# Performance work log

Hardware: AMD Instinct MI355X
Metric: run time of the kernel (lower is better)

The kernel has to match this reference:

```python
import jax, jax.numpy as jnp
import numpy as np

N_NODES = 50000
N_EDGES = 800000
IN_DIM = 128
OUT_DIM = 256


def setup_inputs() -> dict:
    key = jax.random.key(0)
    k1, k2, k3, k4 = jax.random.split(key, 4)
    feat = jax.random.normal(k1, (N_NODES, IN_DIM), dtype=jnp.float32)
    # xavier_uniform with relu gain, shape [in_dim, out_dim] (applied as h @ W)
    gain = np.sqrt(2.0)
    bound = gain * np.sqrt(6.0 / (IN_DIM + OUT_DIM))
    W = jax.random.uniform(k2, (IN_DIM, OUT_DIM), dtype=jnp.float32,
                           minval=-bound, maxval=bound)
    src = jax.random.randint(k3, (N_EDGES,), 0, N_NODES, dtype=jnp.int64)
    dst = jax.random.randint(k4, (N_EDGES,), 0, N_NODES, dtype=jnp.int64)
    return {"feat": feat, "W": W, "src": src, "dst": dst}


def reference(feat, W, src, dst):
    n = feat.shape[0]
    # mean aggregation over incoming neighbors (copy_src + mean on dst)
    msg_sum = jax.ops.segment_sum(feat[src], dst, num_segments=n)  # [N, in_dim]
    deg = jax.ops.segment_sum(jnp.ones_like(dst, dtype=feat.dtype), dst,
                              num_segments=n)  # [N]
    h_neigh = msg_sum / jnp.maximum(deg, 1.0)[:, None]  # zero-degree -> 0
    # self_loop=False path: fc((feat + h_neigh) / 2), then relu
    h = ((feat + h_neigh) * 0.5) @ W  # [N, out_dim]
    return jax.nn.relu(h)
```

## Files before the change

### kernel.cpp

```cpp
#include <hip/hip_runtime.h>
#include <hip/hip_fp16.h>

#define N_NODES 50000
#define N_EDGES 800000
#define IN_DIM  128
#define OUT_DIM 256
#define SCAN_BLOCKS ((N_NODES + 255) / 256)
#define WT_STRIDE 136

typedef _Float16 f16x8 __attribute__((ext_vector_type(8)));
typedef _Float16 f16x4 __attribute__((ext_vector_type(4)));
typedef float f32x4 __attribute__((ext_vector_type(4)));

__global__ void probe_idx_dtype(const int* __restrict__ words,
                                int* __restrict__ flag) {
  __shared__ int cnt;
  if (threadIdx.x == 0) cnt = 0;
  __syncthreads();
  int j = 2 * (int)threadIdx.x + 1;
  if (words[j] != 0) atomicAdd(&cnt, 1);
  __syncthreads();
  if (threadIdx.x == 0) *flag = (cnt == 0) ? 1 : 0;
}

__device__ __forceinline__ long idx_off(long e, int flag) {
  return flag ? (e << 1) : e;
}

__global__ __launch_bounds__(256) void hist_kernel(
    const int* __restrict__ dst, const int* __restrict__ flag,
    int* __restrict__ hist) {
  int e = blockIdx.x * 256 + threadIdx.x;
  if (e >= N_EDGES) return;
  int d = dst[idx_off(e, *flag)];
  atomicAdd(&hist[d], 1);
}

__global__ __launch_bounds__(256) void scan_block(
    const int* __restrict__ hist, int* __restrict__ pre,
    int* __restrict__ bsum) {
  __shared__ int s[256];
  int tid = threadIdx.x;
  int i = blockIdx.x * 256 + tid;
  int v = (i < N_NODES) ? hist[i] : 0;
  s[tid] = v;
  __syncthreads();
  for (int off = 1; off < 256; off <<= 1) {
    int t = (tid >= off) ? s[tid - off] : 0;
    __syncthreads();
    s[tid] += t;
    __syncthreads();
  }
  if (i < N_NODES) pre[i] = s[tid] - v;
  if (tid == 255) bsum[blockIdx.x] = s[255];
}

__global__ __launch_bounds__(256) void scan_tops(int* __restrict__ bsum) {
  __shared__ int s[256];
  int tid = threadIdx.x;
  int v = (tid < SCAN_BLOCKS) ? bsum[tid] : 0;
  s[tid] = v;
  __syncthreads();
  for (int off = 1; off < 256; off <<= 1) {
    int t = (tid >= off) ? s[tid - off] : 0;
    __syncthreads();
    s[tid] += t;
    __syncthreads();
  }
  if (tid < SCAN_BLOCKS) bsum[tid] = s[tid] - v;
}

__global__ __launch_bounds__(256) void scan_add(
    const int* __restrict__ pre, const int* __restrict__ bsum,
    int* __restrict__ row_start) {
  int i = blockIdx.x * 256 + threadIdx.x;
  if (i < N_NODES) row_start[i] = pre[i] + bsum[blockIdx.x];
  if (i == 0) row_start[N_NODES] = N_EDGES;
}

__global__ __launch_bounds__(256) void scatter_kernel(
    const int* __restrict__ src, const int* __restrict__ dst,
    const int* __restrict__ flag, const int* __restrict__ row_start,
    int* __restrict__ cursor, int* __restrict__ esrc) {
  int e = blockIdx.x * 256 + threadIdx.x;
  if (e >= N_EDGES) return;
  int f = *flag;
  int d = dst[idx_off(e, f)];
  int s = src[idx_off(e, f)];
  int pos = row_start[d] + atomicAdd(&cursor[d], 1);
  esrc[pos] = s;
}

__global__ __launch_bounds__(256) void cast_feat(
    const float* __restrict__ feat, __half* __restrict__ feat16) {
  size_t i = ((size_t)blockIdx.x * 256 + threadIdx.x) * 8;
  float4 v0 = *reinterpret_cast<const float4*>(feat + i);
  float4 v1 = *reinterpret_cast<const float4*>(feat + i + 4);
  __half2 h[4];
  h[0] = __floats2half2_rn(v0.x, v0.y);
  h[1] = __floats2half2_rn(v0.z, v0.w);
  h[2] = __floats2half2_rn(v1.x, v1.y);
  h[3] = __floats2half2_rn(v1.z, v1.w);
  *reinterpret_cast<float4*>(feat16 + i) = *reinterpret_cast<float4*>(h);
}

__global__ __launch_bounds__(256) void aggregate_f32(
    const float* __restrict__ feat, const int* __restrict__ esrc,
    const int* __restrict__ row_start, __half2* __restrict__ x) {
  int node = blockIdx.x * 4 + ((int)threadIdx.x >> 6);
  int lane = (int)threadIdx.x & 63;
  if (node >= N_NODES) return;
  int rs = row_start[node];
  int re = row_start[node + 1];
  float2 a0 = {0.f, 0.f}, a1 = {0.f, 0.f};
  int e = rs;
  for (; e + 1 < re; e += 2) {
    int s0 = esrc[e];
    int s1 = esrc[e + 1];
    float2 v0 = *reinterpret_cast<const float2*>(feat + (size_t)s0 * IN_DIM + lane * 2);
    float2 v1 = *reinterpret_cast<const float2*>(feat + (size_t)s1 * IN_DIM + lane * 2);
    a0.x += v0.x; a0.y += v0.y;
    a1.x += v1.x; a1.y += v1.y;
  }
  if (e < re) {
    int s0 = esrc[e];
    float2 v0 = *reinterpret_cast<const float2*>(feat + (size_t)s0 * IN_DIM + lane * 2);
    a0.x += v0.x; a0.y += v0.y;
  }
  float deg = (float)(re - rs);
  float rdeg = (deg > 0.f) ? 1.0f / deg : 0.0f;
  float2 f = *reinterpret_cast<const float2*>(feat + (size_t)node * IN_DIM + lane * 2);
  float x0 = (f.x + (a0.x + a1.x) * rdeg) * 0.5f;
  float x1 = (f.y + (a0.y + a1.y) * rdeg) * 0.5f;
  x[(size_t)node * (IN_DIM / 2) + lane] = __floats2half2_rn(x0, x1);
}

__global__ __launch_bounds__(256) void aggregate_f16(
    const float* __restrict__ feat, const __half* __restrict__ feat16,
    const int* __restrict__ esrc, const int* __restrict__ row_start,
    __half2* __restrict__ x) {
  int node = blockIdx.x * 4 + ((int)threadIdx.x >> 6);
  int lane = (int)threadIdx.x & 63;
  if (node >= N_NODES) return;
  int rs = row_start[node];
  int re = row_start[node + 1];
  float2 a0 = {0.f, 0.f}, a1 = {0.f, 0.f};
  int e = rs;
  for (; e + 1 < re; e += 2) {
    int s0 = esrc[e];
    int s1 = esrc[e + 1];
    __half2 h0 = *reinterpret_cast<const __half2*>(feat16 + (size_t)s0 * IN_DIM + lane * 2);
    __half2 h1 = *reinterpret_cast<const __half2*>(feat16 + (size_t)s1 * IN_DIM + lane * 2);
    float2 v0 = __half22float2(h0);
    float2 v1 = __half22float2(h1);
    a0.x += v0.x; a0.y += v0.y;
    a1.x += v1.x; a1.y += v1.y;
  }
  if (e < re) {
    __half2 h0 = *reinterpret_cast<const __half2*>(feat16 + (size_t)esrc[e] * IN_DIM + lane * 2);
    float2 v0 = __half22float2(h0);
    a0.x += v0.x; a0.y += v0.y;
  }
  float deg = (float)(re - rs);
  float rdeg = (deg > 0.f) ? 1.0f / deg : 0.0f;
  float2 f = *reinterpret_cast<const float2*>(feat + (size_t)node * IN_DIM + lane * 2);
  float x0 = (f.x + (a0.x + a1.x) * rdeg) * 0.5f;
  float x1 = (f.y + (a0.y + a1.y) * rdeg) * 0.5f;
  x[(size_t)node * (IN_DIM / 2) + lane] = __floats2half2_rn(x0, x1);
}

__global__ __launch_bounds__(256) void mfma_gemm(
    const _Float16* __restrict__ x, const float* __restrict__ W,
    float* __restrict__ out) {
  __shared__ _Float16 WT[OUT_DIM * WT_STRIDE];

  const int tid = threadIdx.x;
  {
    const int n = tid;
#pragma unroll
    for (int k = 0; k < IN_DIM; k += 4) {
      f16x4 v;
      v.x = (_Float16)W[(k + 0) * OUT_DIM + n];
      v.y = (_Float16)W[(k + 1) * OUT_DIM + n];
      v.z = (_Float16)W[(k + 2) * OUT_DIM + n];
      v.w = (_Float16)W[(k + 3) * OUT_DIM + n];
      *reinterpret_cast<f16x4*>(&WT[n * WT_STRIDE + k]) = v;
    }
  }
  __syncthreads();

  const int wave = tid >> 6;
  const int lane = tid & 63;
  const int m = lane & 15;
  const int g = lane >> 4;
  const long row_base = (long)blockIdx.x * 128 + wave * 32;

  f16x8 a[2][4];
#pragma unroll
  for (int rt = 0; rt < 2; ++rt) {
    long row = row_base + rt * 16 + m;
#pragma unroll
    for (int kt = 0; kt < 4; ++kt) {
      if (row < N_NODES) {
        a[rt][kt] = *reinterpret_cast<const f16x8*>(
            x + row * IN_DIM + kt * 32 + g * 8);
      } else {
        a[rt][kt] = f16x8{};
      }
    }
  }

#pragma unroll
  for (int nt = 0; nt < 16; ++nt) {
    f16x8 b[4];
#pragma unroll
    for (int kt = 0; kt < 4; ++kt) {
      b[kt] = *reinterpret_cast<const f16x8*>(
          &WT[(nt * 16 + m) * WT_STRIDE + kt * 32 + g * 8]);
    }
    f32x4 acc0 = {0.f, 0.f, 0.f, 0.f};
    f32x4 acc1 = {0.f, 0.f, 0.f, 0.f};
#pragma unroll
    for (int kt = 0; kt < 4; ++kt) {
      acc0 = __builtin_amdgcn_mfma_f32_16x16x32_f16(a[0][kt], b[kt], acc0, 0, 0, 0);
      acc1 = __builtin_amdgcn_mfma_f32_16x16x32_f16(a[1][kt], b[kt], acc1, 0, 0, 0);
    }
    const int col = nt * 16 + m;
#pragma unroll
    for (int j = 0; j < 4; ++j) {
      long r0 = row_base + g * 4 + j;
      long r1 = row_base + 16 + g * 4 + j;
      if (r0 < N_NODES) out[r0 * OUT_DIM + col] = fmaxf(acc0[j], 0.f);
      if (r1 < N_NODES) out[r1 * OUT_DIM + col] = fmaxf(acc1[j], 0.f);
    }
  }
}

extern "C" void kernel_launch(void* const* d_in, const int* in_sizes, int n_in,
                              void* d_out, int out_size, void* d_ws,
                              size_t ws_size, hipStream_t stream) {
  const float* feat = (const float*)d_in[0];
  const float* W = (const float*)d_in[1];
  const int* src = (const int*)d_in[2];
  const int* dst = (const int*)d_in[3];
  float* out = (float*)d_out;

  char* p = (char*)d_ws;
  __half* x = (__half*)p;    p += (size_t)N_NODES * IN_DIM * 2;
  int* esrc = (int*)p;       p += (size_t)N_EDGES * 4;
  int* hist = (int*)p;       p += (size_t)N_NODES * 4;
  int* cursor = (int*)p;     p += (size_t)N_NODES * 4;
  int* pre = (int*)p;        p += (size_t)N_NODES * 4;
  int* row_start = (int*)p;  p += (size_t)(N_NODES + 1) * 4;
  int* bsum = (int*)p;       p += 256 * 4;
  int* flag = (int*)p;       p += 64;
  __half* feat16 = (__half*)p;
  size_t need_f16 = ((char*)feat16 - (char*)d_ws) +
                    (size_t)N_NODES * IN_DIM * 2;
  const bool f16_path = (ws_size >= need_f16);

  hipMemsetAsync(hist, 0, (size_t)2 * N_NODES * 4, stream);

  probe_idx_dtype<<<1, 256, 0, stream>>>(src, flag);

  int eblocks = (N_EDGES + 255) / 256;
  hist_kernel<<<eblocks, 256, 0, stream>>>(dst, flag, hist);
  scan_block<<<SCAN_BLOCKS, 256, 0, stream>>>(hist, pre, bsum);
  scan_tops<<<1, 256, 0, stream>>>(bsum);
  scan_add<<<SCAN_BLOCKS, 256, 0, stream>>>(pre, bsum, row_start);
  scatter_kernel<<<eblocks, 256, 0, stream>>>(src, dst, flag, row_start,
                                              cursor, esrc);
  if (f16_path) {
    cast_feat<<<(N_NODES * IN_DIM) / (256 * 8), 256, 0, stream>>>(feat, feat16);
    aggregate_f16<<<(N_NODES + 3) / 4, 256, 0, stream>>>(feat, feat16, esrc,
                                                         row_start,
                                                         (__half2*)x);
  } else {
    aggregate_f32<<<(N_NODES + 3) / 4, 256, 0, stream>>>(feat, esrc, row_start,
                                                         (__half2*)x);
  }
  mfma_gemm<<<(N_NODES + 127) / 128, 256, 0, stream>>>(
      (const _Float16*)x, W, out);
}
```

Measured before the change: 248.8 us.

## Fuse CSR build stages, cast into histogram, record slots, unroll aggregation

Removes the separate dtype probe kernel by detecting int64 indices inline, and fuses the fp16 feature cast into the histogram kernel. The histogram atomic's return value is saved as a per-edge slot, so the scatter needs no second atomic pass or cursor buffer. The three-kernel scan becomes two by having each block reduce the preceding block sums itself. The f16 aggregation loop is unrolled to four edges, and the GEMM output uses nontemporal stores. The slot array reuses the x buffer, which is safe only because x is written after scatter finishes. The fused cast relies on the node-feature element count (N_NODES*IN_DIM/8) matching N_EDGES exactly.

Result: faster. 210.1 us (-15.6%).

```diff
diff --git a/kernel.cpp b/kernel.cpp
--- a/kernel.cpp
+++ b/kernel.cpp
@@ -12,32 +12,37 @@
 typedef _Float16 f16x4 __attribute__((ext_vector_type(4)));
 typedef float f32x4 __attribute__((ext_vector_type(4)));
 
-__global__ void probe_idx_dtype(const int* __restrict__ words,
-                                int* __restrict__ flag) {
-  __shared__ int cnt;
-  if (threadIdx.x == 0) cnt = 0;
-  __syncthreads();
-  int j = 2 * (int)threadIdx.x + 1;
-  if (words[j] != 0) atomicAdd(&cnt, 1);
-  __syncthreads();
-  if (threadIdx.x == 0) *flag = (cnt == 0) ? 1 : 0;
-}
-
-__device__ __forceinline__ long idx_off(long e, int flag) {
-  return flag ? (e << 1) : e;
-}
-
-__global__ __launch_bounds__(256) void hist_kernel(
-    const int* __restrict__ dst, const int* __restrict__ flag,
-    int* __restrict__ hist) {
-  int e = blockIdx.x * 256 + threadIdx.x;
-  if (e >= N_EDGES) return;
-  int d = dst[idx_off(e, *flag)];
-  atomicAdd(&hist[d], 1);
+__device__ __forceinline__ int detect_i64(const int* __restrict__ idx) {
+  int orv = 0;
+#pragma unroll
+  for (int j = 1; j < 32; j += 2) orv |= idx[j];
+  return orv == 0;
+}
+
+__global__ __launch_bounds__(256) void hist_cast(
+    const int* __restrict__ dst, const float* __restrict__ feat,
+    __half* __restrict__ feat16, int* __restrict__ hist,
+    int* __restrict__ slot) {
+  const int f = detect_i64(dst);
+  const int e = blockIdx.x * 256 + threadIdx.x;
+  const int d = dst[f ? 2 * (long)e : (long)e];
+  slot[e] = atomicAdd(&hist[d], 1);
+
+  if (feat16 != nullptr) {
+    size_t i = (size_t)e * 8;
+    float4 v0 = *reinterpret_cast<const float4*>(feat + i);
+    float4 v1 = *reinterpret_cast<const float4*>(feat + i + 4);
+    __half2 h[4];
+    h[0] = __floats2half2_rn(v0.x, v0.y);
+    h[1] = __floats2half2_rn(v0.z, v0.w);
+    h[2] = __floats2half2_rn(v1.x, v1.y);
+    h[3] = __floats2half2_rn(v1.z, v1.w);
+    *reinterpret_cast<float4*>(feat16 + i) = *reinterpret_cast<float4*>(h);
+  }
 }
 
 __global__ __launch_bounds__(256) void scan_block(
-    const int* __restrict__ hist, int* __restrict__ pre,
+    const int* __restrict__ hist, int* __restrict__ row_start,
     int* __restrict__ bsum) {
   __shared__ int s[256];
   int tid = threadIdx.x;
@@ -51,57 +56,78 @@
     s[tid] += t;
     __syncthreads();
   }
-  if (i < N_NODES) pre[i] = s[tid] - v;
+  if (i < N_NODES) row_start[i] = s[tid] - v;
   if (tid == 255) bsum[blockIdx.x] = s[255];
 }
 
-__global__ __launch_bounds__(256) void scan_tops(int* __restrict__ bsum) {
-  __shared__ int s[256];
+__global__ __launch_bounds__(256) void scan_add(
+    const int* __restrict__ bsum, int* __restrict__ row_start) {
+  __shared__ int sb[256];
   int tid = threadIdx.x;
-  int v = (tid < SCAN_BLOCKS) ? bsum[tid] : 0;
-  s[tid] = v;
+  sb[tid] = (tid < (int)blockIdx.x) ? bsum[tid] : 0;
   __syncthreads();
-  for (int off = 1; off < 256; off <<= 1) {
-    int t = (tid >= off) ? s[tid - off] : 0;
+  for (int off = 128; off > 0; off >>= 1) {
+    if (tid < off) sb[tid] += sb[tid + off];
     __syncthreads();
-    s[tid] += t;
-    __syncthreads();
-  }
-  if (tid < SCAN_BLOCKS) bsum[tid] = s[tid] - v;
-}
-
-__global__ __launch_bounds__(256) void scan_add(
-    const int* __restrict__ pre, const int* __restrict__ bsum,
-    int* __restrict__ row_start) {
-  int i = blockIdx.x * 256 + threadIdx.x;
-  if (i < N_NODES) row_start[i] = pre[i] + bsum[blockIdx.x];
+  }
+  int i = blockIdx.x * 256 + tid;
+  if (i < N_NODES) row_start[i] += sb[0];
   if (i == 0) row_start[N_NODES] = N_EDGES;
 }
 
 __global__ __launch_bounds__(256) void scatter_kernel(
     const int* __restrict__ src, const int* __restrict__ dst,
-    const int* __restrict__ flag, const int* __restrict__ row_start,
-    int* __restrict__ cursor, int* __restrict__ esrc) {
-  int e = blockIdx.x * 256 + threadIdx.x;
-  if (e >= N_EDGES) return;
-  int f = *flag;
-  int d = dst[idx_off(e, f)];
-  int s = src[idx_off(e, f)];
-  int pos = row_start[d] + atomicAdd(&cursor[d], 1);
-  esrc[pos] = s;
-}
-
-__global__ __launch_bounds__(256) void cast_feat(
-    const float* __restrict__ feat, __half* __restrict__ feat16) {
-  size_t i = ((size_t)blockIdx.x * 256 + threadIdx.x) * 8;
-  float4 v0 = *reinterpret_cast<const float4*>(feat + i);
-  float4 v1 = *reinterpret_cast<const float4*>(feat + i + 4);
-  __half2 h[4];
-  h[0] = __floats2half2_rn(v0.x, v0.y);
-  h[1] = __floats2half2_rn(v0.z, v0.w);
-  h[2] = __floats2half2_rn(v1.x, v1.y);
-  h[3] = __floats2half2_rn(v1.z, v1.w);
-  *reinterpret_cast<float4*>(feat16 + i) = *reinterpret_cast<float4*>(h);
+    const int* __restrict__ row_start, const int* __restrict__ slot,
+    int* __restrict__ esrc) {
+  const int f = detect_i64(src);
+  const int e = blockIdx.x * 256 + threadIdx.x;
+  long off = f ? 2 * (long)e : (long)e;
+  int d = dst[off];
+  int s = src[off];
+  esrc[row_start[d] + slot[e]] = s;
+}
+
+__global__ __launch_bounds__(256) void aggregate_f16(
+    const float* __restrict__ feat, const __half* __restrict__ feat16,
+    const int* __restrict__ esrc, const int* __restrict__ row_start,
+    __half2* __restrict__ x) {
+  int node = blockIdx.x * 4 + ((int)threadIdx.x >> 6);
+  int lane = (int)threadIdx.x & 63;
+  if (node >= N_NODES) return;
+  int rs = row_start[node];
+  int re = row_start[node + 1];
+  float2 a0 = {0.f, 0.f}, a1 = {0.f, 0.f}, a2 = {0.f, 0.f}, a3 = {0.f, 0.f};
+  int e = rs;
+  for (; e + 3 < re; e += 4) {
+    int s0 = esrc[e + 0];
+    int s1 = esrc[e + 1];
+    int s2 = esrc[e + 2];
+    int s3 = esrc[e + 3];
+    float2 v0 = __half22float2(*reinterpret_cast<const __half2*>(
+        feat16 + (size_t)s0 * IN_DIM + lane * 2));
+    float2 v1 = __half22float2(*reinterpret_cast<const __half2*>(
+        feat16 + (size_t)s1 * IN_DIM + lane * 2));
+    float2 v2 = __half22float2(*reinterpret_cast<const __half2*>(
+        feat16 + (size_t)s2 * IN_DIM + lane * 2));
+    float2 v3 = __half22float2(*reinterpret_cast<const __half2*>(
+        feat16 + (size_t)s3 * IN_DIM + lane * 2));
+    a0.x += v0.x; a0.y += v0.y;
+    a1.x += v1.x; a1.y += v1.y;
+    a2.x += v2.x; a2.y += v2.y;
+    a3.x += v3.x; a3.y += v3.y;
+  }
+  for (; e < re; ++e) {
+    float2 v0 = __half22float2(*reinterpret_cast<const __half2*>(
+        feat16 + (size_t)esrc[e] * IN_DIM + lane * 2));
+    a0.x += v0.x; a0.y += v0.y;
+  }
+  float deg = (float)(re - rs);
+  float rdeg = (deg > 0.f) ? 1.0f / deg : 0.0f;
+  float2 f = *reinterpret_cast<const float2*>(
+      feat + (size_t)node * IN_DIM + lane * 2);
+  float x0 = (f.x + (a0.x + a1.x + a2.x + a3.x) * rdeg) * 0.5f;
+  float x1 = (f.y + (a0.y + a1.y + a2.y + a3.y) * rdeg) * 0.5f;
+  x[(size_t)node * (IN_DIM / 2) + lane] = __floats2half2_rn(x0, x1);
 }
 
 __global__ __launch_bounds__(256) void aggregate_f32(
@@ -115,55 +141,22 @@
   float2 a0 = {0.f, 0.f}, a1 = {0.f, 0.f};
   int e = rs;
   for (; e + 1 < re; e += 2) {
-    int s0 = esrc[e];
-    int s1 = esrc[e + 1];
-    float2 v0 = *reinterpret_cast<const float2*>(feat + (size_t)s0 * IN_DIM + lane * 2);
-    float2 v1 = *reinterpret_cast<const float2*>(feat + (size_t)s1 * IN_DIM + lane * 2);
+    float2 v0 = *reinterpret_cast<const float2*>(
+        feat + (size_t)esrc[e] * IN_DIM + lane * 2);
+    float2 v1 = *reinterpret_cast<const float2*>(
+        feat + (size_t)esrc[e + 1] * IN_DIM + lane * 2);
     a0.x += v0.x; a0.y += v0.y;
     a1.x += v1.x; a1.y += v1.y;
   }
   if (e < re) {
-    int s0 = esrc[e];
-    float2 v0 = *reinterpret_cast<const float2*>(feat + (size_t)s0 * IN_DIM + lane * 2);
+    float2 v0 = *reinterpret_cast<const float2*>(
+        feat + (size_t)esrc[e] * IN_DIM + lane * 2);
     a0.x += v0.x; a0.y += v0.y;
   }
   float deg = (float)(re - rs);
   float rdeg = (deg > 0.f) ? 1.0f / deg : 0.0f;
-  float2 f = *reinterpret_cast<const float2*>(feat + (size_t)node * IN_DIM + lane * 2);
-  float x0 = (f.x + (a0.x + a1.x) * rdeg) * 0.5f;
-  float x1 = (f.y + (a0.y + a1.y) * rdeg) * 0.5f;
-  x[(size_t)node * (IN_DIM / 2) + lane] = __floats2half2_rn(x0, x1);
-}
-
-__global__ __launch_bounds__(256) void aggregate_f16(
-    const float* __restrict__ feat, const __half* __restrict__ feat16,
-    const int* __restrict__ esrc, const int* __restrict__ row_start,
-    __half2* __restrict__ x) {
-  int node = blockIdx.x * 4 + ((int)threadIdx.x >> 6);
-  int lane = (int)threadIdx.x & 63;
-  if (node >= N_NODES) return;
-  int rs = row_start[node];
-  int re = row_start[node + 1];
-  float2 a0 = {0.f, 0.f}, a1 = {0.f, 0.f};
-  int e = rs;
-  for (; e + 1 < re; e += 2) {
-    int s0 = esrc[e];
-    int s1 = esrc[e + 1];
-    __half2 h0 = *reinterpret_cast<const __half2*>(feat16 + (size_t)s0 * IN_DIM + lane * 2);
-    __half2 h1 = *reinterpret_cast<const __half2*>(feat16 + (size_t)s1 * IN_DIM + lane * 2);
-    float2 v0 = __half22float2(h0);
-    float2 v1 = __half22float2(h1);
-    a0.x += v0.x; a0.y += v0.y;
-    a1.x += v1.x; a1.y += v1.y;
-  }
-  if (e < re) {
-    __half2 h0 = *reinterpret_cast<const __half2*>(feat16 + (size_t)esrc[e] * IN_DIM + lane * 2);
-    float2 v0 = __half22float2(h0);
-    a0.x += v0.x; a0.y += v0.y;
-  }
-  float deg = (float)(re - rs);
-  float rdeg = (deg > 0.f) ? 1.0f / deg : 0.0f;
-  float2 f = *reinterpret_cast<const float2*>(feat + (size_t)node * IN_DIM + lane * 2);
+  float2 f = *reinterpret_cast<const float2*>(
+      feat + (size_t)node * IN_DIM + lane * 2);
   float x0 = (f.x + (a0.x + a1.x) * rdeg) * 0.5f;
   float x1 = (f.y + (a0.y + a1.y) * rdeg) * 0.5f;
   x[(size_t)node * (IN_DIM / 2) + lane] = __floats2half2_rn(x0, x1);
@@ -230,8 +223,12 @@
     for (int j = 0; j < 4; ++j) {
       long r0 = row_base + g * 4 + j;
       long r1 = row_base + 16 + g * 4 + j;
-      if (r0 < N_NODES) out[r0 * OUT_DIM + col] = fmaxf(acc0[j], 0.f);
-      if (r1 < N_NODES) out[r1 * OUT_DIM + col] = fmaxf(acc1[j], 0.f);
+      if (r0 < N_NODES)
+        __builtin_nontemporal_store(fmaxf(acc0[j], 0.f),
+                                    &out[r0 * OUT_DIM + col]);
+      if (r1 < N_NODES)
+        __builtin_nontemporal_store(fmaxf(acc1[j], 0.f),
+                                    &out[r1 * OUT_DIM + col]);
     }
   }
 }
@@ -247,31 +244,27 @@
 
   char* p = (char*)d_ws;
   __half* x = (__half*)p;    p += (size_t)N_NODES * IN_DIM * 2;
+  int* slot = (int*)x;
   int* esrc = (int*)p;       p += (size_t)N_EDGES * 4;
   int* hist = (int*)p;       p += (size_t)N_NODES * 4;
-  int* cursor = (int*)p;     p += (size_t)N_NODES * 4;
-  int* pre = (int*)p;        p += (size_t)N_NODES * 4;
   int* row_start = (int*)p;  p += (size_t)(N_NODES + 1) * 4;
   int* bsum = (int*)p;       p += 256 * 4;
-  int* flag = (int*)p;       p += 64;
+  p = (char*)(((uintptr_t)p + 15) & ~(uintptr_t)15);
   __half* feat16 = (__half*)p;
-  size_t need_f16 = ((char*)feat16 - (char*)d_ws) +
-                    (size_t)N_NODES * IN_DIM * 2;
+  size_t need_f16 =
+      ((char*)feat16 - (char*)d_ws) + (size_t)N_NODES * IN_DIM * 2;
   const bool f16_path = (ws_size >= need_f16);
 
-  hipMemsetAsync(hist, 0, (size_t)2 * N_NODES * 4, stream);
-
-  probe_idx_dtype<<<1, 256, 0, stream>>>(src, flag);
-
-  int eblocks = (N_EDGES + 255) / 256;
-  hist_kernel<<<eblocks, 256, 0, stream>>>(dst, flag, hist);
-  scan_block<<<SCAN_BLOCKS, 256, 0, stream>>>(hist, pre, bsum);
-  scan_tops<<<1, 256, 0, stream>>>(bsum);
-  scan_add<<<SCAN_BLOCKS, 256, 0, stream>>>(pre, bsum, row_start);
-  scatter_kernel<<<eblocks, 256, 0, stream>>>(src, dst, flag, row_start,
-                                              cursor, esrc);
+  hipMemsetAsync(hist, 0, (size_t)N_NODES * 4, stream);
+
+  const int eblocks = N_EDGES / 256;
+  hist_cast<<<eblocks, 256, 0, stream>>>(dst, feat,
+                                         f16_path ? feat16 : nullptr, hist,
+                                         slot);
+  scan_block<<<SCAN_BLOCKS, 256, 0, stream>>>(hist, row_start, bsum);
+  scan_add<<<SCAN_BLOCKS, 256, 0, stream>>>(bsum, row_start);
+  scatter_kernel<<<eblocks, 256, 0, stream>>>(src, dst, row_start, slot, esrc);
   if (f16_path) {
-    cast_feat<<<(N_NODES * IN_DIM) / (256 * 8), 256, 0, stream>>>(feat, feat16);
     aggregate_f16<<<(N_NODES + 3) / 4, 256, 0, stream>>>(feat, feat16, esrc,
                                                          row_start,
                                                          (__half2*)x);
```
